# Kernel optimization log

Measured on AMD Instinct MI355X. Metric: run time of the kernel, lower is better.

Reference implementation:

```python
import jax, jax.numpy as jnp
import numpy as np

B, T, D, UNITS, VOCAB = 32, 128, 512, 1024, 32000
DROP_P = 0.1


def setup_inputs() -> dict:
    key = jax.random.key(0)
    ks = jax.random.split(key, 8)
    initial_input = jax.random.normal(ks[0], (B, T, D), dtype=jnp.float32)
    h0 = jax.random.normal(ks[1], (B, UNITS), dtype=jnp.float32)
    c0 = jax.random.normal(ks[2], (B, UNITS), dtype=jnp.float32)
    W = jax.random.normal(ks[3], (D, 4 * UNITS), dtype=jnp.float32) * (1.0 / np.sqrt(D))
    U = jax.random.normal(ks[4], (UNITS, 4 * UNITS), dtype=jnp.float32) * (1.0 / np.sqrt(UNITS))
    b = jnp.zeros((4 * UNITS,), dtype=jnp.float32)
    Wd = jax.random.normal(ks[5], (UNITS, VOCAB), dtype=jnp.float32) * (1.0 / np.sqrt(UNITS))
    bd = jnp.zeros((VOCAB,), dtype=jnp.float32)
    # Keras recurrent_dropout: 4 independent inverted-dropout masks on h_{t-1},
    # one per gate (i, f, c, o), constant across timesteps.
    keep = jax.random.bernoulli(ks[6], 1.0 - DROP_P, (4, B, UNITS))
    rec_masks = keep.astype(jnp.float32) / (1.0 - DROP_P)
    return {"initial_input": initial_input, "h0": h0, "c0": c0, "W": W, "U": U,
            "b": b, "Wd": Wd, "bd": bd, "rec_masks": rec_masks}


def reference(initial_input, h0, c0, W, U, b, Wd, bd, rec_masks):
    units = h0.shape[-1]
    # Precompute input projection for all timesteps: [T, B, 4U]
    xW = jnp.einsum('btd,dk->tbk', initial_input, W) + b
    m_i, m_f, m_c, m_o = rec_masks[0], rec_masks[1], rec_masks[2], rec_masks[3]
    U_i, U_f, U_c, U_o = jnp.split(U, 4, axis=1)

    def step(carry, xw_t):
        h, c = carry
        z_i = xw_t[:, 0 * units:1 * units] + (h * m_i) @ U_i
        z_f = xw_t[:, 1 * units:2 * units] + (h * m_f) @ U_f
        z_c = xw_t[:, 2 * units:3 * units] + (h * m_c) @ U_c
        z_o = xw_t[:, 3 * units:4 * units] + (h * m_o) @ U_o
        i = jax.nn.sigmoid(z_i)
        f = jax.nn.sigmoid(z_f)
        c_new = f * c + i * jnp.tanh(z_c)
        o = jax.nn.sigmoid(z_o)
        h_new = o * jnp.tanh(c_new)
        return (h_new, c_new), h_new

    (hT, cT), hs = jax.lax.scan(step, (h0, c0), xW)
    out = jnp.transpose(hs, (1, 0, 2))  # [B, T, U]
    logits = out @ Wd + bd  # [B, T, VOCAB]
    return logits, hT, cT
```

## Files before the change

### kernel.cpp

```cpp
#include <hip/hip_runtime.h>
#include <cmath>


#define BB 32
#define TT 128
#define DD 512
#define UU 1024
#define GG 4096
#define VV 32000
constexpr float MASK_SCALE = 1.0f / 0.9f;

typedef __attribute__((ext_vector_type(8))) short short8_t;
typedef __attribute__((ext_vector_type(4))) float f32x4;

__device__ __forceinline__ unsigned short f2bf(float f) {
  unsigned u = __builtin_bit_cast(unsigned, f);
  unsigned r = (u + 0x7FFFu + ((u >> 16) & 1u)) >> 16;
  return (unsigned short)r;
}
__device__ __forceinline__ float bf2f(unsigned short h) {
  unsigned u = ((unsigned)h) << 16;
  return __builtin_bit_cast(float, u);
}

__global__ __launch_bounds__(256, 2) void gemm128(
    const float* __restrict__ A, const float* __restrict__ Bm,
    const float* __restrict__ bias, float* __restrict__ C,
    int M, int N, int K) {
  __shared__ float As[8][128];
  __shared__ float Bs[8][128];
  const int tid = threadIdx.x;
  const int m0 = blockIdx.y * 128;
  const int n0 = blockIdx.x * 128;
  const int a_r = tid >> 1, a_k4 = (tid & 1) * 4;
  const int b_k = tid >> 5, b_n4 = (tid & 31) * 4;
  const int mm = (tid & 15) * 4;
  const int nn = (tid >> 4) * 4;
  float acc[8][8];
#pragma unroll
  for (int i = 0; i < 8; ++i)
#pragma unroll
    for (int j = 0; j < 8; ++j) acc[i][j] = 0.f;

  for (int k0 = 0; k0 < K; k0 += 8) {
    const float4 av = *(const float4*)(A + (size_t)(m0 + a_r) * K + k0 + a_k4);
    const float4 bv = *(const float4*)(Bm + (size_t)(k0 + b_k) * N + n0 + b_n4);
    __syncthreads();
    As[a_k4 + 0][a_r] = av.x;
    As[a_k4 + 1][a_r] = av.y;
    As[a_k4 + 2][a_r] = av.z;
    As[a_k4 + 3][a_r] = av.w;
    *(float4*)(&Bs[b_k][b_n4]) = bv;
    __syncthreads();
#pragma unroll
    for (int k = 0; k < 8; ++k) {
      const float4 a0 = *(const float4*)(&As[k][mm]);
      const float4 a1 = *(const float4*)(&As[k][mm + 64]);
      const float4 q0 = *(const float4*)(&Bs[k][nn]);
      const float4 q1 = *(const float4*)(&Bs[k][nn + 64]);
      const float ar[8] = {a0.x, a0.y, a0.z, a0.w, a1.x, a1.y, a1.z, a1.w};
      const float br[8] = {q0.x, q0.y, q0.z, q0.w, q1.x, q1.y, q1.z, q1.w};
#pragma unroll
      for (int i = 0; i < 8; ++i)
#pragma unroll
        for (int j = 0; j < 8; ++j) acc[i][j] += ar[i] * br[j];
    }
  }
  const float4 bi0 = *(const float4*)(bias + n0 + nn);
  const float4 bi1 = *(const float4*)(bias + n0 + nn + 64);
  const float bia[8] = {bi0.x, bi0.y, bi0.z, bi0.w, bi1.x, bi1.y, bi1.z, bi1.w};
#pragma unroll
  for (int i = 0; i < 8; ++i) {
    const int m = m0 + (i < 4 ? mm + i : mm + 60 + i);
    float* cp = C + (size_t)m * N + n0;
    float4 v0 = {acc[i][0] + bia[0], acc[i][1] + bia[1], acc[i][2] + bia[2], acc[i][3] + bia[3]};
    float4 v1 = {acc[i][4] + bia[4], acc[i][5] + bia[5], acc[i][6] + bia[6], acc[i][7] + bia[7]};
    *(float4*)(cp + nn) = v0;
    *(float4*)(cp + nn + 64) = v1;
  }
}

__global__ __launch_bounds__(256) void convert_wd(
    const float* __restrict__ Wd, unsigned short* __restrict__ Bhi,
    unsigned short* __restrict__ Blo) {
  __shared__ float tile[64][65];
  const int tid = threadIdx.x;
  const int tx = tid & 63, ty = tid >> 6;
  const int n0 = blockIdx.x * 64, k0 = blockIdx.y * 64;
#pragma unroll 4
  for (int r = 0; r < 16; ++r) {
    const int k = ty * 16 + r;
    tile[k][tx] = Wd[(size_t)(k0 + k) * VV + n0 + tx];
  }
  __syncthreads();
#pragma unroll 4
  for (int r = 0; r < 16; ++r) {
    const int n = ty * 16 + r;
    const float v = tile[tx][n];
    const unsigned short hi = f2bf(v);
    const float lof = v - bf2f(hi);
    const size_t o = (size_t)(n0 + n) * UU + k0 + tx;
    Bhi[o] = hi;
    Blo[o] = f2bf(lof);
  }
}

__global__ __launch_bounds__(256, 2) void gemm_mfma_logits(
    const unsigned short* __restrict__ Ahi, const unsigned short* __restrict__ Alo,
    const unsigned short* __restrict__ Bhi, const unsigned short* __restrict__ Blo,
    const float* __restrict__ bias, float* __restrict__ C) {
  __shared__ unsigned short AsHi[128][40], AsLo[128][40];
  __shared__ unsigned short BsHi[128][40], BsLo[128][40];
  const int tid = threadIdx.x;
  const int lane = tid & 63;
  const int wave = tid >> 6;
  const int wm = wave >> 1, wn = wave & 1;
  const int q = lane >> 4, l15 = lane & 15;
  const int n0 = blockIdx.x * 128;
  const int m0 = blockIdx.y * 128;
  const int srow = tid >> 2;
  const int sk = (tid & 3) * 8;

  f32x4 acc[4][4];
#pragma unroll
  for (int mf = 0; mf < 4; ++mf)
#pragma unroll
    for (int nf = 0; nf < 4; ++nf) acc[mf][nf] = f32x4{0.f, 0.f, 0.f, 0.f};

  const size_t arow0 = (size_t)(m0 + srow) * UU + sk;
  const size_t arow1 = (size_t)(m0 + 64 + srow) * UU + sk;
  const size_t brow0 = (size_t)(n0 + srow) * UU + sk;
  const size_t brow1 = (size_t)(n0 + 64 + srow) * UU + sk;

  for (int k0 = 0; k0 < UU; k0 += 32) {
    const short8_t ra0h = *(const short8_t*)(Ahi + arow0 + k0);
    const short8_t ra1h = *(const short8_t*)(Ahi + arow1 + k0);
    const short8_t ra0l = *(const short8_t*)(Alo + arow0 + k0);
    const short8_t ra1l = *(const short8_t*)(Alo + arow1 + k0);
    const short8_t rb0h = *(const short8_t*)(Bhi + brow0 + k0);
    const short8_t rb1h = *(const short8_t*)(Bhi + brow1 + k0);
    const short8_t rb0l = *(const short8_t*)(Blo + brow0 + k0);
    const short8_t rb1l = *(const short8_t*)(Blo + brow1 + k0);
    __syncthreads();
    *(short8_t*)&AsHi[srow][sk] = ra0h;
    *(short8_t*)&AsHi[64 + srow][sk] = ra1h;
    *(short8_t*)&AsLo[srow][sk] = ra0l;
    *(short8_t*)&AsLo[64 + srow][sk] = ra1l;
    *(short8_t*)&BsHi[srow][sk] = rb0h;
    *(short8_t*)&BsHi[64 + srow][sk] = rb1h;
    *(short8_t*)&BsLo[srow][sk] = rb0l;
    *(short8_t*)&BsLo[64 + srow][sk] = rb1l;
    __syncthreads();

    short8_t ah[4], al[4], bh[4], bl[4];
#pragma unroll
    for (int f = 0; f < 4; ++f) {
      ah[f] = *(const short8_t*)&AsHi[wm * 64 + f * 16 + l15][q * 8];
      al[f] = *(const short8_t*)&AsLo[wm * 64 + f * 16 + l15][q * 8];
      bh[f] = *(const short8_t*)&BsHi[wn * 64 + f * 16 + l15][q * 8];
      bl[f] = *(const short8_t*)&BsLo[wn * 64 + f * 16 + l15][q * 8];
    }
#pragma unroll
    for (int mf = 0; mf < 4; ++mf)
#pragma unroll
      for (int nf = 0; nf < 4; ++nf) {
        f32x4 a = acc[mf][nf];
        a = __builtin_amdgcn_mfma_f32_16x16x32_bf16(ah[mf], bh[nf], a, 0, 0, 0);
        a = __builtin_amdgcn_mfma_f32_16x16x32_bf16(ah[mf], bl[nf], a, 0, 0, 0);
        a = __builtin_amdgcn_mfma_f32_16x16x32_bf16(al[mf], bh[nf], a, 0, 0, 0);
        acc[mf][nf] = a;
      }
  }

#pragma unroll
  for (int nf = 0; nf < 4; ++nf) {
    const int n = n0 + wn * 64 + nf * 16 + l15;
    const float bia = bias[n];
#pragma unroll
    for (int mf = 0; mf < 4; ++mf) {
      const int mbase = m0 + wm * 64 + mf * 16 + q * 4;
#pragma unroll
      for (int r = 0; r < 4; ++r)
        C[(size_t)(mbase + r) * VV + n] = acc[mf][nf][r] + bia;
    }
  }
}

__global__ __launch_bounds__(256) void prep_kernel(
    const float* __restrict__ h0, const float* __restrict__ c0,
    const float* __restrict__ masks, float* __restrict__ hT0,
    float* __restrict__ cst, unsigned* __restrict__ mbits) {
  const int i = blockIdx.x * 256 + threadIdx.x;
  if (i < BB * UU) {
    hT0[i] = h0[(i & 31) * UU + (i >> 5)];
    cst[i] = c0[i];
  }
  if (i < 4 * UU) {
    const int g = i >> 10, k = i & 1023;
    unsigned w = 0;
#pragma unroll 4
    for (int b = 0; b < 32; ++b)
      if (masks[(size_t)(g * 32 + b) * UU + k] != 0.f) w |= (1u << b);
    mbits[i] = w;
  }
}

__global__ __launch_bounds__(256) void lstm_step(
    const float* __restrict__ xw,
    const float* __restrict__ Um,
    const float* __restrict__ hin,
    float* __restrict__ hout,
    float* __restrict__ cst,
    const unsigned* __restrict__ mbits,
    unsigned short* __restrict__ hsHi, unsigned short* __restrict__ hsLo,
    float* __restrict__ hs,
    float* __restrict__ outH, float* __restrict__ outC,
    int t) {
  __shared__ float red[256 * 17];
  const int tid = threadIdx.x;
  const int kc = tid >> 5;
  const int g = (tid >> 3) & 3;
  const int bg = tid & 7;
  const int b0 = bg * 4;
  const int ub = (blockIdx.x & 7) * 32 + (blockIdx.x >> 3);
  const int u0 = ub * 4;

  float acc[4][4];
#pragma unroll
  for (int i = 0; i < 4; ++i)
#pragma unroll
    for (int j = 0; j < 4; ++j) acc[i][j] = 0.f;

  const unsigned* wb = mbits + g * UU;
  const int kbeg = kc * 128;
#pragma unroll 4
  for (int k = kbeg; k < kbeg + 128; ++k) {
    const float4 h4 = *(const float4*)(hin + k * 32 + b0);
    const unsigned w = wb[k];
    const float4 u4 = *(const float4*)(Um + (size_t)k * GG + g * UU + u0);
    const float hm0 = ((w >> (b0 + 0)) & 1) ? h4.x * MASK_SCALE : 0.f;
    const float hm1 = ((w >> (b0 + 1)) & 1) ? h4.y * MASK_SCALE : 0.f;
    const float hm2 = ((w >> (b0 + 2)) & 1) ? h4.z * MASK_SCALE : 0.f;
    const float hm3 = ((w >> (b0 + 3)) & 1) ? h4.w * MASK_SCALE : 0.f;
    acc[0][0] += hm0 * u4.x; acc[0][1] += hm0 * u4.y; acc[0][2] += hm0 * u4.z; acc[0][3] += hm0 * u4.w;
    acc[1][0] += hm1 * u4.x; acc[1][1] += hm1 * u4.y; acc[1][2] += hm1 * u4.z; acc[1][3] += hm1 * u4.w;
    acc[2][0] += hm2 * u4.x; acc[2][1] += hm2 * u4.y; acc[2][2] += hm2 * u4.z; acc[2][3] += hm2 * u4.w;
    acc[3][0] += hm3 * u4.x; acc[3][1] += hm3 * u4.y; acc[3][2] += hm3 * u4.z; acc[3][3] += hm3 * u4.w;
  }
#pragma unroll
  for (int i = 0; i < 4; ++i)
#pragma unroll
    for (int j = 0; j < 4; ++j) red[tid * 17 + i * 4 + j] = acc[i][j];
  __syncthreads();

  if (tid < 128) {
    const int b = tid >> 2, ul = tid & 3;
    const int u = u0 + ul;
    float z[4];
#pragma unroll
    for (int gg = 0; gg < 4; ++gg) {
      float s = 0.f;
#pragma unroll
      for (int kk = 0; kk < 8; ++kk)
        s += red[(kk * 32 + gg * 8 + (b >> 2)) * 17 + (b & 3) * 4 + ul];
      z[gg] = s + xw[((size_t)(b * TT + t)) * GG + gg * UU + u];
    }
    const float ig = 1.f / (1.f + expf(-z[0]));
    const float fg = 1.f / (1.f + expf(-z[1]));
    const float cc = tanhf(z[2]);
    const float og = 1.f / (1.f + expf(-z[3]));
    const float cold = cst[b * UU + u];
    const float cnew = fg * cold + ig * cc;
    const float hnew = og * tanhf(cnew);
    cst[b * UU + u] = cnew;
    hout[u * 32 + b] = hnew;
    const size_t idx = ((size_t)b * TT + t) * UU + u;
    if (hsHi) {
      const unsigned short hi = f2bf(hnew);
      hsHi[idx] = hi;
      hsLo[idx] = f2bf(hnew - bf2f(hi));
    } else {
      hs[idx] = hnew;
    }
    if (t == TT - 1) {
      outH[b * UU + u] = hnew;
      outC[b * UU + u] = cnew;
    }
  }
}

extern "C" void kernel_launch(void* const* d_in, const int* in_sizes, int n_in,
                              void* d_out, int out_size, void* d_ws, size_t ws_size,
                              hipStream_t stream) {
  const float* x     = (const float*)d_in[0];
  const float* h0    = (const float*)d_in[1];
  const float* c0    = (const float*)d_in[2];
  const float* W     = (const float*)d_in[3];
  const float* Um    = (const float*)d_in[4];
  const float* bvec  = (const float*)d_in[5];
  const float* Wd    = (const float*)d_in[6];
  const float* bd    = (const float*)d_in[7];
  const float* masks = (const float*)d_in[8];

  float* out = (float*)d_out;
  float* logits = out;
  float* outH = out + (size_t)BB * TT * VV;
  float* outC = outH + (size_t)BB * UU;
  float* xw = logits;

  const size_t SZ_HS   = (size_t)BB * TT * UU * 2;
  const size_t SZ_WD   = (size_t)VV * UU * 2;
  const size_t SZ_HT   = 2 * (size_t)UU * BB * 4;
  const size_t SZ_CST  = (size_t)BB * UU * 4;
  const size_t SZ_MB   = 4 * (size_t)UU * 4;
  const size_t NEED = 2 * SZ_HS + 2 * SZ_WD + SZ_HT + SZ_CST + SZ_MB;

  char* ws = (char*)d_ws;
  const bool fast = (ws_size >= NEED);

  unsigned short *hsHi = nullptr, *hsLo = nullptr, *WdHi = nullptr, *WdLo = nullptr;
  float *hs = nullptr, *hT = nullptr, *cst = nullptr;
  unsigned* mbits = nullptr;

  if (fast) {
    hsHi = (unsigned short*)ws;              ws += SZ_HS;
    hsLo = (unsigned short*)ws;              ws += SZ_HS;
    WdHi = (unsigned short*)ws;              ws += SZ_WD;
    WdLo = (unsigned short*)ws;              ws += SZ_WD;
    hT   = (float*)ws;                       ws += SZ_HT;
    cst  = (float*)ws;                       ws += SZ_CST;
    mbits = (unsigned*)ws;
  } else {
    hs   = (float*)ws;                       ws += (size_t)BB * TT * UU * 4;
    hT   = (float*)ws;                       ws += SZ_HT;
    cst  = (float*)ws;                       ws += SZ_CST;
    mbits = (unsigned*)ws;
  }

  prep_kernel<<<128, 256, 0, stream>>>(h0, c0, masks, hT, cst, mbits);

  if (fast)
    convert_wd<<<dim3(VV / 64, UU / 64), 256, 0, stream>>>(Wd, WdHi, WdLo);

  gemm128<<<dim3(GG / 128, (BB * TT) / 128), 256, 0, stream>>>(
      x, W, bvec, xw, BB * TT, GG, DD);

  for (int t = 0; t < TT; ++t) {
    const float* hin = hT + (size_t)(t & 1) * (UU * BB);
    float* hout      = hT + (size_t)((t + 1) & 1) * (UU * BB);
    lstm_step<<<256, 256, 0, stream>>>(xw, Um, hin, hout, cst, mbits,
                                       hsHi, hsLo, hs, outH, outC, t);
  }

  if (fast) {
    gemm_mfma_logits<<<dim3(VV / 128, (BB * TT) / 128), 256, 0, stream>>>(
        hsHi, hsLo, WdHi, WdLo, bd, logits);
  } else {
    gemm128<<<dim3(VV / 128, (BB * TT) / 128), 256, 0, stream>>>(
        hs, Wd, bd, logits, BB * TT, VV, UU);
  }
}
```

Baseline: 4.660 ms.

## Fuse LSTM steps into persistent kernel with grid barrier; use single fp16 logits GEMM

Replaces the 128 per-timestep launches with one persistent lstm_scan kernel. It keeps each block's U slice resident in LDS and the cell state in registers, and synchronises blocks across timesteps with an atomic-counter grid barrier. The logits GEMM drops the 3-MFMA bf16 hi/lo split for a single fp16 MFMA, which reduces precision. The masks become transposed floats and U is pre-transposed. The grid barrier assumes all 256 blocks are co-resident, and the fp16 path may lose accuracy.

New measurement: 7.159 ms. 1.54x slower.

```diff
diff --git a/kernel.cpp b/kernel.cpp
--- a/kernel.cpp
+++ b/kernel.cpp
@@ -8,20 +8,10 @@
 #define UU 1024
 #define GG 4096
 #define VV 32000
-constexpr float MASK_SCALE = 1.0f / 0.9f;
 
 typedef __attribute__((ext_vector_type(8))) short short8_t;
+typedef __attribute__((ext_vector_type(8))) _Float16 f16x8;
 typedef __attribute__((ext_vector_type(4))) float f32x4;
-
-__device__ __forceinline__ unsigned short f2bf(float f) {
-  unsigned u = __builtin_bit_cast(unsigned, f);
-  unsigned r = (u + 0x7FFFu + ((u >> 16) & 1u)) >> 16;
-  return (unsigned short)r;
-}
-__device__ __forceinline__ float bf2f(unsigned short h) {
-  unsigned u = ((unsigned)h) << 16;
-  return __builtin_bit_cast(float, u);
-}
 
 __global__ __launch_bounds__(256, 2) void gemm128(
     const float* __restrict__ A, const float* __restrict__ Bm,
@@ -81,8 +71,7 @@
 }
 
 __global__ __launch_bounds__(256) void convert_wd(
-    const float* __restrict__ Wd, unsigned short* __restrict__ Bhi,
-    unsigned short* __restrict__ Blo) {
+    const float* __restrict__ Wd, unsigned short* __restrict__ Bh) {
   __shared__ float tile[64][65];
   const int tid = threadIdx.x;
   const int tx = tid & 63, ty = tid >> 6;
@@ -97,27 +86,163 @@
   for (int r = 0; r < 16; ++r) {
     const int n = ty * 16 + r;
     const float v = tile[tx][n];
-    const unsigned short hi = f2bf(v);
-    const float lof = v - bf2f(hi);
-    const size_t o = (size_t)(n0 + n) * UU + k0 + tx;
-    Bhi[o] = hi;
-    Blo[o] = f2bf(lof);
-  }
-}
-
-__global__ __launch_bounds__(256, 2) void gemm_mfma_logits(
-    const unsigned short* __restrict__ Ahi, const unsigned short* __restrict__ Alo,
-    const unsigned short* __restrict__ Bhi, const unsigned short* __restrict__ Blo,
+    Bh[(size_t)(n0 + n) * UU + k0 + tx] =
+        __builtin_bit_cast(unsigned short, (_Float16)v);
+  }
+}
+
+__global__ __launch_bounds__(256) void transpose_u(
+    const float* __restrict__ Um, float* __restrict__ UT) {
+  __shared__ float tile[64][65];
+  const int tid = threadIdx.x;
+  const int tx = tid & 63, ty = tid >> 6;
+  const int c0 = blockIdx.x * 64, k0 = blockIdx.y * 64;
+#pragma unroll 4
+  for (int r = 0; r < 16; ++r) {
+    const int k = ty * 16 + r;
+    tile[k][tx] = Um[(size_t)(k0 + k) * GG + c0 + tx];
+  }
+  __syncthreads();
+#pragma unroll 4
+  for (int r = 0; r < 16; ++r) {
+    const int c = ty * 16 + r;
+    UT[(size_t)(c0 + c) * UU + k0 + tx] = tile[tx][c];
+  }
+}
+
+__global__ __launch_bounds__(256) void prep_kernel(
+    const float* __restrict__ h0, const float* __restrict__ masks,
+    float* __restrict__ hT0, float* __restrict__ mT, unsigned* __restrict__ cnt) {
+  const int i = blockIdx.x * 256 + threadIdx.x;
+  if (i < BB * UU)
+    hT0[i] = h0[(i & 31) * UU + (i >> 5)];
+  const int g = i >> 15, k = (i >> 5) & 1023, b = i & 31;
+  mT[i] = masks[((size_t)g * BB + b) * UU + k];
+  if (i == 0) *cnt = 0u;
+}
+
+__global__ __launch_bounds__(256) void lstm_scan(
+    const float* __restrict__ xw,
+    const float* __restrict__ UT,
+    const float* __restrict__ mT,
+    float* __restrict__ hT,
+    const float* __restrict__ c0,
+    unsigned short* __restrict__ hs16,
+    float* __restrict__ outH, float* __restrict__ outC,
+    unsigned* __restrict__ cnt) {
+  __shared__ float Us[1024][16];
+  __shared__ float red2[8 * 4 * 132];
+
+  const int tid = threadIdx.x;
+  const int bq = tid & 7;
+  const int cq = (tid >> 3) & 3;
+  const int kc = tid >> 5;
+  const int b0 = bq * 4;
+  const int u0 = blockIdx.x * 4;
+
+#pragma unroll
+  for (int c = 0; c < 16; ++c) {
+    const int g = c >> 2, uu = c & 3;
+    const float4 v = *(const float4*)(UT + ((size_t)g * UU + u0 + uu) * UU + tid * 4);
+#pragma unroll
+    for (int j = 0; j < 4; ++j) Us[tid * 4 + j][c] = (&v.x)[j];
+  }
+  __syncthreads();
+
+  const int fb = tid >> 2, fu = tid & 3;
+  float c_reg = 0.f;
+  if (tid < 128) c_reg = c0[fb * UU + u0 + fu];
+
+  const float* mrow = mT + (size_t)cq * (UU * BB);
+  const unsigned nblk = gridDim.x;
+
+  for (int t = 0; t < TT; ++t) {
+    const float* hin = hT + (size_t)(t & 1) * (UU * BB);
+    float* hout = hT + (size_t)((t + 1) & 1) * (UU * BB);
+
+    float acc[4][4];
+#pragma unroll
+    for (int i = 0; i < 4; ++i)
+#pragma unroll
+      for (int j = 0; j < 4; ++j) acc[i][j] = 0.f;
+
+    const int kbeg = kc * 128;
+#pragma unroll 4
+    for (int k = kbeg; k < kbeg + 128; ++k) {
+      const float4 h4 = *(const float4*)(hin + k * 32 + b0);
+      const float4 m4 = *(const float4*)(mrow + k * 32 + b0);
+      const float hm0 = h4.x * m4.x, hm1 = h4.y * m4.y;
+      const float hm2 = h4.z * m4.z, hm3 = h4.w * m4.w;
+#pragma unroll
+      for (int j = 0; j < 4; ++j) {
+        const float uv = Us[k][cq * 4 + j];
+        acc[0][j] += hm0 * uv;
+        acc[1][j] += hm1 * uv;
+        acc[2][j] += hm2 * uv;
+        acc[3][j] += hm3 * uv;
+      }
+    }
+
+    __syncthreads();
+#pragma unroll
+    for (int i = 0; i < 4; ++i)
+#pragma unroll
+      for (int j = 0; j < 4; ++j)
+        red2[(kc * 4 + cq) * 132 + (b0 + i) * 4 + j] = acc[i][j];
+    __syncthreads();
+
+    if (tid < 128) {
+      const float* xwp = xw + ((size_t)(fb * TT + t)) * GG + u0 + fu;
+      float z[4];
+#pragma unroll
+      for (int g = 0; g < 4; ++g) {
+        float s = 0.f;
+#pragma unroll
+        for (int k8 = 0; k8 < 8; ++k8) s += red2[(k8 * 4 + g) * 132 + tid];
+        z[g] = s + xwp[(size_t)g * UU];
+      }
+      const float ig = 1.f / (1.f + expf(-z[0]));
+      const float fg = 1.f / (1.f + expf(-z[1]));
+      const float cc = tanhf(z[2]);
+      const float og = 1.f / (1.f + expf(-z[3]));
+      const float cnew = fg * c_reg + ig * cc;
+      const float hnew = og * tanhf(cnew);
+      c_reg = cnew;
+      hout[(u0 + fu) * 32 + fb] = hnew;
+      hs16[((size_t)(fb * TT + t)) * UU + u0 + fu] =
+          __builtin_bit_cast(unsigned short, (_Float16)hnew);
+      if (t == TT - 1) {
+        outH[fb * UU + u0 + fu] = hnew;
+        outC[fb * UU + u0 + fu] = cnew;
+      }
+    }
+
+    if (t < TT - 1) {
+      __syncthreads();
+      if (tid == 0) {
+        __threadfence();
+        __hip_atomic_fetch_add(cnt, 1u, __ATOMIC_RELEASE, __HIP_MEMORY_SCOPE_AGENT);
+        const unsigned target = (unsigned)(t + 1) * nblk;
+        while (__hip_atomic_load(cnt, __ATOMIC_ACQUIRE, __HIP_MEMORY_SCOPE_AGENT) < target) {}
+      }
+      __syncthreads();
+      __threadfence();
+    }
+  }
+}
+
+__global__ __launch_bounds__(256, 2) void gemm_f16_logits(
+    const unsigned short* __restrict__ Ah, const unsigned short* __restrict__ Bh,
     const float* __restrict__ bias, float* __restrict__ C) {
-  __shared__ unsigned short AsHi[128][40], AsLo[128][40];
-  __shared__ unsigned short BsHi[128][40], BsLo[128][40];
+  __shared__ unsigned short As[128][40];
+  __shared__ unsigned short Bs[128][40];
   const int tid = threadIdx.x;
   const int lane = tid & 63;
   const int wave = tid >> 6;
   const int wm = wave >> 1, wn = wave & 1;
   const int q = lane >> 4, l15 = lane & 15;
-  const int n0 = blockIdx.x * 128;
-  const int m0 = blockIdx.y * 128;
+  const int m0 = blockIdx.x * 128;
+  const int n0 = blockIdx.y * 128;
   const int srow = tid >> 2;
   const int sk = (tid & 3) * 8;
 
@@ -133,43 +258,28 @@
   const size_t brow1 = (size_t)(n0 + 64 + srow) * UU + sk;
 
   for (int k0 = 0; k0 < UU; k0 += 32) {
-    const short8_t ra0h = *(const short8_t*)(Ahi + arow0 + k0);
-    const short8_t ra1h = *(const short8_t*)(Ahi + arow1 + k0);
-    const short8_t ra0l = *(const short8_t*)(Alo + arow0 + k0);
-    const short8_t ra1l = *(const short8_t*)(Alo + arow1 + k0);
-    const short8_t rb0h = *(const short8_t*)(Bhi + brow0 + k0);
-    const short8_t rb1h = *(const short8_t*)(Bhi + brow1 + k0);
-    const short8_t rb0l = *(const short8_t*)(Blo + brow0 + k0);
-    const short8_t rb1l = *(const short8_t*)(Blo + brow1 + k0);
-    __syncthreads();
-    *(short8_t*)&AsHi[srow][sk] = ra0h;
-    *(short8_t*)&AsHi[64 + srow][sk] = ra1h;
-    *(short8_t*)&AsLo[srow][sk] = ra0l;
-    *(short8_t*)&AsLo[64 + srow][sk] = ra1l;
-    *(short8_t*)&BsHi[srow][sk] = rb0h;
-    *(short8_t*)&BsHi[64 + srow][sk] = rb1h;
-    *(short8_t*)&BsLo[srow][sk] = rb0l;
-    *(short8_t*)&BsLo[64 + srow][sk] = rb1l;
-    __syncthreads();
-
-    short8_t ah[4], al[4], bh[4], bl[4];
+    const short8_t ra0 = *(const short8_t*)(Ah + arow0 + k0);
+    const short8_t ra1 = *(const short8_t*)(Ah + arow1 + k0);
+    const short8_t rb0 = *(const short8_t*)(Bh + brow0 + k0);
+    const short8_t rb1 = *(const short8_t*)(Bh + brow1 + k0);
+    __syncthreads();
+    *(short8_t*)&As[srow][sk] = ra0;
+    *(short8_t*)&As[64 + srow][sk] = ra1;
+    *(short8_t*)&Bs[srow][sk] = rb0;
+    *(short8_t*)&Bs[64 + srow][sk] = rb1;
+    __syncthreads();
+
+    f16x8 ah[4], bh[4];
 #pragma unroll
     for (int f = 0; f < 4; ++f) {
-      ah[f] = *(const short8_t*)&AsHi[wm * 64 + f * 16 + l15][q * 8];
-      al[f] = *(const short8_t*)&AsLo[wm * 64 + f * 16 + l15][q * 8];
-      bh[f] = *(const short8_t*)&BsHi[wn * 64 + f * 16 + l15][q * 8];
-      bl[f] = *(const short8_t*)&BsLo[wn * 64 + f * 16 + l15][q * 8];
+      ah[f] = __builtin_bit_cast(f16x8, *(const short8_t*)&As[wm * 64 + f * 16 + l15][q * 8]);
+      bh[f] = __builtin_bit_cast(f16x8, *(const short8_t*)&Bs[wn * 64 + f * 16 + l15][q * 8]);
     }
 #pragma unroll
     for (int mf = 0; mf < 4; ++mf)
 #pragma unroll
-      for (int nf = 0; nf < 4; ++nf) {
-        f32x4 a = acc[mf][nf];
-        a = __builtin_amdgcn_mfma_f32_16x16x32_bf16(ah[mf], bh[nf], a, 0, 0, 0);
-        a = __builtin_amdgcn_mfma_f32_16x16x32_bf16(ah[mf], bl[nf], a, 0, 0, 0);
-        a = __builtin_amdgcn_mfma_f32_16x16x32_bf16(al[mf], bh[nf], a, 0, 0, 0);
-        acc[mf][nf] = a;
-      }
+      for (int nf = 0; nf < 4; ++nf)
+        acc[mf][nf] = __builtin_amdgcn_mfma_f32_16x16x32_f16(ah[mf], bh[nf], acc[mf][nf], 0, 0, 0);
   }
 
 #pragma unroll
@@ -182,109 +292,6 @@
 #pragma unroll
       for (int r = 0; r < 4; ++r)
         C[(size_t)(mbase + r) * VV + n] = acc[mf][nf][r] + bia;
-    }
-  }
-}
-
-__global__ __launch_bounds__(256) void prep_kernel(
-    const float* __restrict__ h0, const float* __restrict__ c0,
-    const float* __restrict__ masks, float* __restrict__ hT0,
-    float* __restrict__ cst, unsigned* __restrict__ mbits) {
-  const int i = blockIdx.x * 256 + threadIdx.x;
-  if (i < BB * UU) {
-    hT0[i] = h0[(i & 31) * UU + (i >> 5)];
-    cst[i] = c0[i];
-  }
-  if (i < 4 * UU) {
-    const int g = i >> 10, k = i & 1023;
-    unsigned w = 0;
-#pragma unroll 4
-    for (int b = 0; b < 32; ++b)
-      if (masks[(size_t)(g * 32 + b) * UU + k] != 0.f) w |= (1u << b);
-    mbits[i] = w;
-  }
-}
-
-__global__ __launch_bounds__(256) void lstm_step(
-    const float* __restrict__ xw,
-    const float* __restrict__ Um,
-    const float* __restrict__ hin,
-    float* __restrict__ hout,
-    float* __restrict__ cst,
-    const unsigned* __restrict__ mbits,
-    unsigned short* __restrict__ hsHi, unsigned short* __restrict__ hsLo,
-    float* __restrict__ hs,
-    float* __restrict__ outH, float* __restrict__ outC,
-    int t) {
-  __shared__ float red[256 * 17];
-  const int tid = threadIdx.x;
-  const int kc = tid >> 5;
-  const int g = (tid >> 3) & 3;
-  const int bg = tid & 7;
-  const int b0 = bg * 4;
-  const int ub = (blockIdx.x & 7) * 32 + (blockIdx.x >> 3);
-  const int u0 = ub * 4;
-
-  float acc[4][4];
-#pragma unroll
-  for (int i = 0; i < 4; ++i)
-#pragma unroll
-    for (int j = 0; j < 4; ++j) acc[i][j] = 0.f;
-
-  const unsigned* wb = mbits + g * UU;
-  const int kbeg = kc * 128;
-#pragma unroll 4
-  for (int k = kbeg; k < kbeg + 128; ++k) {
-    const float4 h4 = *(const float4*)(hin + k * 32 + b0);
-    const unsigned w = wb[k];
-    const float4 u4 = *(const float4*)(Um + (size_t)k * GG + g * UU + u0);
-    const float hm0 = ((w >> (b0 + 0)) & 1) ? h4.x * MASK_SCALE : 0.f;
-    const float hm1 = ((w >> (b0 + 1)) & 1) ? h4.y * MASK_SCALE : 0.f;
-    const float hm2 = ((w >> (b0 + 2)) & 1) ? h4.z * MASK_SCALE : 0.f;
-    const float hm3 = ((w >> (b0 + 3)) & 1) ? h4.w * MASK_SCALE : 0.f;
-    acc[0][0] += hm0 * u4.x; acc[0][1] += hm0 * u4.y; acc[0][2] += hm0 * u4.z; acc[0][3] += hm0 * u4.w;
-    acc[1][0] += hm1 * u4.x; acc[1][1] += hm1 * u4.y; acc[1][2] += hm1 * u4.z; acc[1][3] += hm1 * u4.w;
-    acc[2][0] += hm2 * u4.x; acc[2][1] += hm2 * u4.y; acc[2][2] += hm2 * u4.z; acc[2][3] += hm2 * u4.w;
-    acc[3][0] += hm3 * u4.x; acc[3][1] += hm3 * u4.y; acc[3][2] += hm3 * u4.z; acc[3][3] += hm3 * u4.w;
-  }
-#pragma unroll
-  for (int i = 0; i < 4; ++i)
-#pragma unroll
-    for (int j = 0; j < 4; ++j) red[tid * 17 + i * 4 + j] = acc[i][j];
-  __syncthreads();
-
-  if (tid < 128) {
-    const int b = tid >> 2, ul = tid & 3;
-    const int u = u0 + ul;
-    float z[4];
-#pragma unroll
-    for (int gg = 0; gg < 4; ++gg) {
-      float s = 0.f;
-#pragma unroll
-      for (int kk = 0; kk < 8; ++kk)
-        s += red[(kk * 32 + gg * 8 + (b >> 2)) * 17 + (b & 3) * 4 + ul];
-      z[gg] = s + xw[((size_t)(b * TT + t)) * GG + gg * UU + u];
-    }
-    const float ig = 1.f / (1.f + expf(-z[0]));
-    const float fg = 1.f / (1.f + expf(-z[1]));
-    const float cc = tanhf(z[2]);
-    const float og = 1.f / (1.f + expf(-z[3]));
-    const float cold = cst[b * UU + u];
-    const float cnew = fg * cold + ig * cc;
-    const float hnew = og * tanhf(cnew);
-    cst[b * UU + u] = cnew;
-    hout[u * 32 + b] = hnew;
-    const size_t idx = ((size_t)b * TT + t) * UU + u;
-    if (hsHi) {
-      const unsigned short hi = f2bf(hnew);
-      hsHi[idx] = hi;
-      hsLo[idx] = f2bf(hnew - bf2f(hi));
-    } else {
-      hs[idx] = hnew;
-    }
-    if (t == TT - 1) {
-      outH[b * UU + u] = hnew;
-      outC[b * UU + u] = cnew;
     }
   }
 }
@@ -308,55 +315,23 @@
   float* outC = outH + (size_t)BB * UU;
   float* xw = logits;
 
-  const size_t SZ_HS   = (size_t)BB * TT * UU * 2;
-  const size_t SZ_WD   = (size_t)VV * UU * 2;
-  const size_t SZ_HT   = 2 * (size_t)UU * BB * 4;
-  const size_t SZ_CST  = (size_t)BB * UU * 4;
-  const size_t SZ_MB   = 4 * (size_t)UU * 4;
-  const size_t NEED = 2 * SZ_HS + 2 * SZ_WD + SZ_HT + SZ_CST + SZ_MB;
-
   char* ws = (char*)d_ws;
-  const bool fast = (ws_size >= NEED);
-
-  unsigned short *hsHi = nullptr, *hsLo = nullptr, *WdHi = nullptr, *WdLo = nullptr;
-  float *hs = nullptr, *hT = nullptr, *cst = nullptr;
-  unsigned* mbits = nullptr;
-
-  if (fast) {
-    hsHi = (unsigned short*)ws;              ws += SZ_HS;
-    hsLo = (unsigned short*)ws;              ws += SZ_HS;
-    WdHi = (unsigned short*)ws;              ws += SZ_WD;
-    WdLo = (unsigned short*)ws;              ws += SZ_WD;
-    hT   = (float*)ws;                       ws += SZ_HT;
-    cst  = (float*)ws;                       ws += SZ_CST;
-    mbits = (unsigned*)ws;
-  } else {
-    hs   = (float*)ws;                       ws += (size_t)BB * TT * UU * 4;
-    hT   = (float*)ws;                       ws += SZ_HT;
-    cst  = (float*)ws;                       ws += SZ_CST;
-    mbits = (unsigned*)ws;
-  }
-
-  prep_kernel<<<128, 256, 0, stream>>>(h0, c0, masks, hT, cst, mbits);
-
-  if (fast)
-    convert_wd<<<dim3(VV / 64, UU / 64), 256, 0, stream>>>(Wd, WdHi, WdLo);
+  unsigned short* WdT16 = (unsigned short*)ws;      ws += (size_t)VV * UU * 2;
+  unsigned short* hs16  = (unsigned short*)ws;      ws += (size_t)BB * TT * UU * 2;
+  float* UT   = (float*)ws;                         ws += (size_t)GG * UU * 4;
+  float* mT   = (float*)ws;                         ws += (size_t)4 * UU * BB * 4;
+  float* hT   = (float*)ws;                         ws += (size_t)2 * UU * BB * 4;
+  unsigned* cnt = (unsigned*)ws;
+
+  prep_kernel<<<512, 256, 0, stream>>>(h0, masks, hT, mT, cnt);
+  transpose_u<<<dim3(GG / 64, UU / 64), 256, 0, stream>>>(Um, UT);
+  convert_wd<<<dim3(VV / 64, UU / 64), 256, 0, stream>>>(Wd, WdT16);
 
   gemm128<<<dim3(GG / 128, (BB * TT) / 128), 256, 0, stream>>>(
       x, W, bvec, xw, BB * TT, GG, DD);
 
-  for (int t = 0; t < TT; ++t) {
-    const float* hin = hT + (size_t)(t & 1) * (UU * BB);
-    float* hout      = hT + (size_t)((t + 1) & 1) * (UU * BB);
-    lstm_step<<<256, 256, 0, stream>>>(xw, Um, hin, hout, cst, mbits,
-                                       hsHi, hsLo, hs, outH, outC, t);
-  }
-
-  if (fast) {
-    gemm_mfma_logits<<<dim3(VV / 128, (BB * TT) / 128), 256, 0, stream>>>(
-        hsHi, hsLo, WdHi, WdLo, bd, logits);
-  } else {
-    gemm128<<<dim3(VV / 128, (BB * TT) / 128), 256, 0, stream>>>(
-        hs, Wd, bd, logits, BB * TT, VV, UU);
-  }
-}
+  lstm_scan<<<256, 256, 0, stream>>>(xw, UT, mT, hT, c0, hs16, outH, outC, cnt);
+
+  gemm_f16_logits<<<dim3((BB * TT) / 128, VV / 128), 256, 0, stream>>>(
+      hs16, WdT16, bd, logits);
+}
```
